# Performance work log

Hardware: AMD Instinct MI355X
Metric: run time of the kernel (lower is better)

Reference implementation:

```python
import jax, jax.numpy as jnp
import numpy as np

N_PATIENT = 50000
N_GENE = 20000
N_EDGE = 640000
P_DIM, G_DIM, H, OUT = 64, 32, 128, 8


def setup_inputs() -> dict:
    key = jax.random.key(0)
    ks = jax.random.split(key, 20)
    s = 0.02
    return {
        "x_patient": jax.random.normal(ks[0], (N_PATIENT, P_DIM), jnp.float32),
        "x_gene": jax.random.normal(ks[1], (N_GENE, G_DIM), jnp.float32),
        "edge_index": jax.random.randint(ks[2], (2, N_EDGE), 0, N_GENE, jnp.int32),
        # patient MLP
        "W_p1": jax.random.normal(ks[3], (P_DIM, H), jnp.float32) * s,
        "b_p1": jnp.zeros((H,), jnp.float32),
        "W_p2": jax.random.normal(ks[4], (H, H), jnp.float32) * s,
        "b_p2": jnp.zeros((H,), jnp.float32),
        # gene MLP
        "W_g1": jax.random.normal(ks[5], (G_DIM, H), jnp.float32) * s,
        "b_g1": jnp.zeros((H,), jnp.float32),
        "W_g2": jax.random.normal(ks[6], (H, H), jnp.float32) * s,
        "b_g2": jnp.zeros((H,), jnp.float32),
        # SAGEConv 1: lin_l acts on aggregated src, lin_r (root) on dst
        "W1_l": jax.random.normal(ks[7], (H, H), jnp.float32) * s,
        "b1_l": jnp.zeros((H,), jnp.float32),
        "W1_r": jax.random.normal(ks[8], (H, H), jnp.float32) * s,
        # SAGEConv 2
        "W2_l": jax.random.normal(ks[9], (H, H), jnp.float32) * s,
        "b2_l": jnp.zeros((H,), jnp.float32),
        "W2_r": jax.random.normal(ks[10], (H, H), jnp.float32) * s,
        # final fc
        "W_fc": jax.random.normal(ks[11], (H, OUT), jnp.float32) * s,
        "b_fc": jnp.zeros((OUT,), jnp.float32),
    }


def reference(x_patient, x_gene, edge_index,
              W_p1, b_p1, W_p2, b_p2,
              W_g1, b_g1, W_g2, b_g2,
              W1_l, b1_l, W1_r,
              W2_l, b2_l, W2_r,
              W_fc, b_fc):
    # node-type MLPs
    p = jax.nn.relu(x_patient @ W_p1 + b_p1) @ W_p2 + b_p2   # [N_P, H]
    g = jax.nn.relu(x_gene @ W_g1 + b_g1) @ W_g2 + b_g2       # [N_G, H]

    src, dst = edge_index[0], edge_index[1]
    # gene_x is unchanged between layers, so the sum-aggregate is identical
    # for both SAGEConv layers: compute the gather + segment-sum once.
    agg = jax.ops.segment_sum(g[src], dst, num_segments=x_patient.shape[0])  # [N_P, H]

    # SAGEConv(aggr='sum'): out = lin_l(agg) + lin_r(x_dst), bias in lin_l
    p = jax.nn.relu(agg @ W1_l + b1_l + p @ W1_r)
    p = jax.nn.relu(agg @ W2_l + b2_l + p @ W2_r)
    return p @ W_fc + b_fc  # [N_P, OUT]
```

## Files before the change

### kernel.cpp

```cpp
#include <hip/hip_runtime.h>

#define NP 50000
#define NG 20000
#define NE 640000
#define PD 64
#define GD 32
#define HD 128
#define OD 8
#define CAP 96
#define FILLB 125
#define EPB 5120
#define GENE_TILES 313
#define ROW0_NOAGG 20096
#define PAT2B 234
#define SAGE64B 314

using f32x4 = __attribute__((ext_vector_type(4))) float;
using s16x8 = __attribute__((ext_vector_type(8))) short;

__device__ __forceinline__ unsigned short f2bf(float f) {
    union { float f; unsigned u; } v; v.f = f;
    const unsigned r = v.u + 0x7FFFu + ((v.u >> 16) & 1u);
    return (unsigned short)(r >> 16);
}
__device__ __forceinline__ float bfpair_lo(unsigned v) {
    union { unsigned u; float f; } x; x.u = v << 16; return x.f;
}
__device__ __forceinline__ float bfpair_hi(unsigned v) {
    union { unsigned u; float f; } x; x.u = v & 0xFFFF0000u; return x.f;
}

#define TOT_SWZ 112640

__global__ __launch_bounds__(256) void swz_kernel(
    const float* __restrict__ Wp1, const float* __restrict__ Wp2,
    const float* __restrict__ W1l, const float* __restrict__ W1r,
    const float* __restrict__ W2l, const float* __restrict__ W2r,
    const float* __restrict__ Wfc,
    const float* __restrict__ Wg1, const float* __restrict__ Wg2,
    unsigned short* __restrict__ wswz)
{
    const int u = blockIdx.x * 256 + threadIdx.x;
    if (u < TOT_SWZ) {
        const float* src; int K, Nr, doff;
        if      (u <   8192) { src = Wp1; K =  64; Nr = HD; doff = 0; }
        else if (u <  24576) { src = Wp2; K = 128; Nr = HD; doff = 8192; }
        else if (u <  40960) { src = W1l; K = 128; Nr = HD; doff = 24576; }
        else if (u <  57344) { src = W1r; K = 128; Nr = HD; doff = 40960; }
        else if (u <  73728) { src = W2l; K = 128; Nr = HD; doff = 57344; }
        else if (u <  90112) { src = W2r; K = 128; Nr = HD; doff = 73728; }
        else if (u <  92160) { src = Wfc; K = 128; Nr = OD; doff = 90112; }
        else if (u <  96256) { src = Wg1; K =  32; Nr = HD; doff = 92160; }
        else                 { src = Wg2; K = 128; Nr = HD; doff = 96256; }
        const int e  = u - doff;
        const int j  = e & 7;
        const int ln = (e >> 3) & 63;
        const int f  = e >> 9;
        const int KC = K >> 5;
        const int c  = f % KC;
        const int n0 = f / KC;
        const int k  = c * 32 + (ln >> 4) * 8 + j;
        const int n  = n0 * 16 + (ln & 15);
        wswz[u] = f2bf((n < Nr) ? src[k * Nr + n] : 0.f);
    }
}

__global__ __launch_bounds__(256) void mega_kernel(
    const float* __restrict__ xp, const float* __restrict__ xg,
    const unsigned short* __restrict__ wswz,
    const float* __restrict__ bg1, const float* __restrict__ bg2,
    const float* __restrict__ bp1, const float* __restrict__ bp2,
    const float* __restrict__ b1l, const float* __restrict__ b2l,
    const float* __restrict__ bfc,
    const int* __restrict__ ei,
    unsigned short* __restrict__ g, int* __restrict__ hist,
    float* __restrict__ out)
{
    __shared__ __align__(16) char smem[40960];
    const int bid = blockIdx.x;
    const int tid = threadIdx.x;

    if (bid >= PAT2B + GENE_TILES) {
        int* cnt = (int*)smem;
#pragma unroll
        for (int k = 0; k < 10; ++k) {
            const int idx = k * 256 + tid;
            if (idx < NG / 8) ((int4*)cnt)[idx] = (int4){0, 0, 0, 0};
        }
        __syncthreads();
        const int fb = bid - PAT2B - GENE_TILES;
        const int base = fb * EPB;
#pragma unroll
        for (int it = 0; it < 5; ++it) {
            const int e0 = base + it * 1024 + tid;
            const int d0 = ei[NE + e0];
            const int d1 = ei[NE + e0 + 256];
            const int d2 = ei[NE + e0 + 512];
            const int d3 = ei[NE + e0 + 768];
            atomicAdd(&cnt[d0 >> 1], 1 << ((d0 & 1) * 16));
            atomicAdd(&cnt[d1 >> 1], 1 << ((d1 & 1) * 16));
            atomicAdd(&cnt[d2 >> 1], 1 << ((d2 & 1) * 16));
            atomicAdd(&cnt[d3 >> 1], 1 << ((d3 & 1) * 16));
        }
        __syncthreads();
        int* Hb = hist + fb * NG;
#pragma unroll
        for (int k = 0; k < 40; ++k) {
            const int idx = k * 256 + tid;
            if (idx < NG / 2) {
                const unsigned w = (unsigned)cnt[idx];
                ((int2*)Hb)[idx] = (int2){(int)(w & 0xFFFFu), (int)(w >> 16)};
            }
        }
        return;
    }

    const int lane = tid & 63;
    const int wid  = tid >> 6;
    const int quad = lane >> 4;
    const int l16  = lane & 15;
    const f32x4 Z = {0.f, 0.f, 0.f, 0.f};

    if (bid >= PAT2B) {
        const unsigned short* wg1 = wswz + 92160;
        const unsigned short* wg2 = wswz + 96256;
        const int row0 = (bid - PAT2B) * 64 + wid * 16;
        const int arow = min(row0 + l16, NG - 1);
        unsigned short* X = (unsigned short*)smem + wid * 16 * 136;

        s16x8 a;
        {
            const float* xr = xg + (size_t)arow * GD + quad * 8;
            const f32x4 u0 = *(const f32x4*)xr;
            const f32x4 u1 = *(const f32x4*)(xr + 4);
#pragma unroll
            for (int j = 0; j < 4; ++j) {
                a[j]     = (short)f2bf(u0[j]);
                a[4 + j] = (short)f2bf(u1[j]);
            }
        }
        f32x4 C[8];
#pragma unroll
        for (int n = 0; n < 8; ++n) {
            const s16x8 b = *(const s16x8*)&wg1[(n * 64 + lane) * 8];
            C[n] = __builtin_amdgcn_mfma_f32_16x16x32_bf16(a, b, Z, 0, 0, 0);
        }
#pragma unroll
        for (int n = 0; n < 8; ++n) {
            const float bias = bg1[n * 16 + l16];
#pragma unroll
            for (int r = 0; r < 4; ++r)
                X[(quad * 4 + r) * 136 + n * 16 + l16] = f2bf(fmaxf(C[n][r] + bias, 0.f));
        }
        __syncthreads();
        s16x8 pa[4];
#pragma unroll
        for (int c = 0; c < 4; ++c) pa[c] = *(const s16x8*)&X[l16 * 136 + c * 32 + quad * 8];
#pragma unroll
        for (int n = 0; n < 8; ++n) {
            C[n] = Z;
#pragma unroll
            for (int c = 0; c < 4; ++c) {
                const s16x8 b = *(const s16x8*)&wg2[((n * 4 + c) * 64 + lane) * 8];
                C[n] = __builtin_amdgcn_mfma_f32_16x16x32_bf16(pa[c], b, C[n], 0, 0, 0);
            }
        }
#pragma unroll
        for (int n = 0; n < 8; ++n) {
            const float bias = bg2[n * 16 + l16];
#pragma unroll
            for (int r = 0; r < 4; ++r) {
                const int row = row0 + quad * 4 + r;
                if (row < NG) g[(size_t)row * HD + n * 16 + l16] = f2bf(C[n][r] + bias);
            }
        }
        return;
    }

    const unsigned short* wp1 = wswz + 0;
    const unsigned short* wp2 = wswz + 8192;
    const unsigned short* w1r = wswz + 40960;
    const unsigned short* w2r = wswz + 73728;
    const unsigned short* wfc = wswz + 90112;

    unsigned short* XA = (unsigned short*)smem;
    const int brow = ROW0_NOAGG + bid * 128;
    const int nA = wid * 2, nB = wid * 2 + 1;

#pragma unroll
    for (int s = 0; s < 8; ++s) {
        const int slot = s * 256 + tid;
        const int r  = slot >> 4;
        const int cv = slot & 15;
        const f32x4 u = *(const f32x4*)&xp[(size_t)min(brow + r, NP - 1) * PD + cv * 4];
        unsigned short o[4];
#pragma unroll
        for (int j = 0; j < 4; ++j) o[j] = f2bf(u[j]);
        *(ushort4*)&XA[r * 136 + cv * 4] = *(ushort4*)o;
    }
    __syncthreads();

    f32x4 acc[8][2];

#pragma unroll
    for (int rt = 0; rt < 8; ++rt) { acc[rt][0] = Z; acc[rt][1] = Z; }
#pragma unroll
    for (int c = 0; c < 2; ++c) {
        const s16x8 b0 = *(const s16x8*)&wp1[((nA * 2 + c) * 64 + lane) * 8];
        const s16x8 b1 = *(const s16x8*)&wp1[((nB * 2 + c) * 64 + lane) * 8];
#pragma unroll
        for (int rt = 0; rt < 8; ++rt) {
            const s16x8 a = *(const s16x8*)&XA[(rt * 16 + l16) * 136 + c * 32 + quad * 8];
            acc[rt][0] = __builtin_amdgcn_mfma_f32_16x16x32_bf16(a, b0, acc[rt][0], 0, 0, 0);
            acc[rt][1] = __builtin_amdgcn_mfma_f32_16x16x32_bf16(a, b1, acc[rt][1], 0, 0, 0);
        }
    }
    __syncthreads();
#pragma unroll
    for (int t = 0; t < 2; ++t) {
        const int n = wid * 2 + t;
        const float bias = bp1[n * 16 + l16];
#pragma unroll
        for (int rt = 0; rt < 8; ++rt)
#pragma unroll
            for (int r = 0; r < 4; ++r)
                XA[(rt * 16 + quad * 4 + r) * 136 + n * 16 + l16] =
                    f2bf(fmaxf(acc[rt][t][r] + bias, 0.f));
    }
    __syncthreads();

#pragma unroll
    for (int rt = 0; rt < 8; ++rt) { acc[rt][0] = Z; acc[rt][1] = Z; }
#pragma unroll
    for (int c = 0; c < 4; ++c) {
        const s16x8 b0 = *(const s16x8*)&wp2[((nA * 4 + c) * 64 + lane) * 8];
        const s16x8 b1 = *(const s16x8*)&wp2[((nB * 4 + c) * 64 + lane) * 8];
#pragma unroll
        for (int rt = 0; rt < 8; ++rt) {
            const s16x8 a = *(const s16x8*)&XA[(rt * 16 + l16) * 136 + c * 32 + quad * 8];
            acc[rt][0] = __builtin_amdgcn_mfma_f32_16x16x32_bf16(a, b0, acc[rt][0], 0, 0, 0);
            acc[rt][1] = __builtin_amdgcn_mfma_f32_16x16x32_bf16(a, b1, acc[rt][1], 0, 0, 0);
        }
    }
    __syncthreads();
#pragma unroll
    for (int t = 0; t < 2; ++t) {
        const int n = wid * 2 + t;
        const float bias = bp2[n * 16 + l16];
#pragma unroll
        for (int rt = 0; rt < 8; ++rt)
#pragma unroll
            for (int r = 0; r < 4; ++r)
                XA[(rt * 16 + quad * 4 + r) * 136 + n * 16 + l16] =
                    f2bf(acc[rt][t][r] + bias);
    }
    __syncthreads();

#pragma unroll
    for (int rt = 0; rt < 8; ++rt) { acc[rt][0] = Z; acc[rt][1] = Z; }
#pragma unroll
    for (int c = 0; c < 4; ++c) {
        const s16x8 b0 = *(const s16x8*)&w1r[((nA * 4 + c) * 64 + lane) * 8];
        const s16x8 b1 = *(const s16x8*)&w1r[((nB * 4 + c) * 64 + lane) * 8];
#pragma unroll
        for (int rt = 0; rt < 8; ++rt) {
            const s16x8 a = *(const s16x8*)&XA[(rt * 16 + l16) * 136 + c * 32 + quad * 8];
            acc[rt][0] = __builtin_amdgcn_mfma_f32_16x16x32_bf16(a, b0, acc[rt][0], 0, 0, 0);
            acc[rt][1] = __builtin_amdgcn_mfma_f32_16x16x32_bf16(a, b1, acc[rt][1], 0, 0, 0);
        }
    }
    __syncthreads();
#pragma unroll
    for (int t = 0; t < 2; ++t) {
        const int n = wid * 2 + t;
        const float bias = b1l[n * 16 + l16];
#pragma unroll
        for (int rt = 0; rt < 8; ++rt)
#pragma unroll
            for (int r = 0; r < 4; ++r)
                XA[(rt * 16 + quad * 4 + r) * 136 + n * 16 + l16] =
                    f2bf(fmaxf(acc[rt][t][r] + bias, 0.f));
    }
    __syncthreads();

#pragma unroll
    for (int rt = 0; rt < 8; ++rt) { acc[rt][0] = Z; acc[rt][1] = Z; }
#pragma unroll
    for (int c = 0; c < 4; ++c) {
        const s16x8 b0 = *(const s16x8*)&w2r[((nA * 4 + c) * 64 + lane) * 8];
        const s16x8 b1 = *(const s16x8*)&w2r[((nB * 4 + c) * 64 + lane) * 8];
#pragma unroll
        for (int rt = 0; rt < 8; ++rt) {
            const s16x8 a = *(const s16x8*)&XA[(rt * 16 + l16) * 136 + c * 32 + quad * 8];
            acc[rt][0] = __builtin_amdgcn_mfma_f32_16x16x32_bf16(a, b0, acc[rt][0], 0, 0, 0);
            acc[rt][1] = __builtin_amdgcn_mfma_f32_16x16x32_bf16(a, b1, acc[rt][1], 0, 0, 0);
        }
    }
    __syncthreads();
#pragma unroll
    for (int t = 0; t < 2; ++t) {
        const int n = wid * 2 + t;
        const float bias = b2l[n * 16 + l16];
#pragma unroll
        for (int rt = 0; rt < 8; ++rt)
#pragma unroll
            for (int r = 0; r < 4; ++r)
                XA[(rt * 16 + quad * 4 + r) * 136 + n * 16 + l16] =
                    f2bf(fmaxf(acc[rt][t][r] + bias, 0.f));
    }
    __syncthreads();

    {
        f32x4 co[2] = {Z, Z};
#pragma unroll
        for (int c = 0; c < 4; ++c) {
            const s16x8 b = *(const s16x8*)&wfc[(c * 64 + lane) * 8];
#pragma unroll
            for (int j = 0; j < 2; ++j) {
                const int rt = wid * 2 + j;
                const s16x8 a = *(const s16x8*)&XA[(rt * 16 + l16) * 136 + c * 32 + quad * 8];
                co[j] = __builtin_amdgcn_mfma_f32_16x16x32_bf16(a, b, co[j], 0, 0, 0);
            }
        }
        if (l16 < OD) {
            const float bias = bfc[l16];
#pragma unroll
            for (int j = 0; j < 2; ++j)
#pragma unroll
                for (int r = 0; r < 4; ++r) {
                    const int row = brow + (wid * 2 + j) * 16 + quad * 4 + r;
                    if (row < NP) out[(size_t)row * OD + l16] = co[j][r] + bias;
                }
        }
    }
}

__global__ __launch_bounds__(256) void scan_kernel(
    int* __restrict__ hist, int* __restrict__ cursor)
{
    const int d = blockIdx.x * 256 + threadIdx.x;
    if (d >= NG) return;
    int run = 0;
#pragma unroll 5
    for (int b = 0; b < FILLB; ++b) {
        const int t = hist[b * NG + d];
        hist[b * NG + d] = run;
        run += t;
    }
    cursor[d] = run;
}

__global__ __launch_bounds__(256) void place_kernel(
    const int* __restrict__ ei, const int* __restrict__ hist,
    unsigned short* __restrict__ pad)
{
    __shared__ __align__(16) int cnt[NG];
    const int tid = threadIdx.x;
    const int* Hb = hist + blockIdx.x * NG;
#pragma unroll
    for (int k = 0; k < 20; ++k) {
        const int idx = k * 256 + tid;
        if (idx < NG / 4) ((int4*)cnt)[idx] = ((const int4*)Hb)[idx];
    }
    __syncthreads();
    const int base = blockIdx.x * EPB;
#pragma unroll
    for (int it = 0; it < 5; ++it) {
        const int e0 = base + it * 1024 + tid;
        const int s0 = ei[e0];       const int d0 = ei[NE + e0];
        const int s1 = ei[e0 + 256]; const int d1 = ei[NE + e0 + 256];
        const int s2 = ei[e0 + 512]; const int d2 = ei[NE + e0 + 512];
        const int s3 = ei[e0 + 768]; const int d3 = ei[NE + e0 + 768];
        { const int p = atomicAdd(&cnt[d0], 1); if (p < CAP) pad[d0 * CAP + p] = (unsigned short)s0; }
        { const int p = atomicAdd(&cnt[d1], 1); if (p < CAP) pad[d1 * CAP + p] = (unsigned short)s1; }
        { const int p = atomicAdd(&cnt[d2], 1); if (p < CAP) pad[d2 * CAP + p] = (unsigned short)s2; }
        { const int p = atomicAdd(&cnt[d3], 1); if (p < CAP) pad[d3 * CAP + p] = (unsigned short)s3; }
    }
}

__global__ __launch_bounds__(256) void agg_kernel(
    const int* __restrict__ cursor, const unsigned short* __restrict__ pad,
    const unsigned short* __restrict__ g, unsigned short* __restrict__ aggb)
{
    const int row  = blockIdx.x * 4 + (threadIdx.x >> 6);
    const int lane = threadIdx.x & 63;
    const int grp  = lane >> 4;
    const int sub  = lane & 15;

    float acc[8] = {0.f, 0.f, 0.f, 0.f, 0.f, 0.f, 0.f, 0.f};
    const int cnt = min(cursor[row], CAP);
    const size_t rb = (size_t)row * CAP;
    for (int i = grp * 4; i < cnt; i += 16) {
        const ushort4 q = *(const ushort4*)&pad[rb + i];
        int r0 = q.x, r1 = q.y, r2 = q.z, r3 = q.w;
        const bool v1 = (i + 1) < cnt, v2 = (i + 2) < cnt, v3 = (i + 3) < cnt;
        r1 = v1 ? r1 : r0;  r2 = v2 ? r2 : r0;  r3 = v3 ? r3 : r0;
        const float s1 = v1 ? 1.f : 0.f, s2 = v2 ? 1.f : 0.f, s3 = v3 ? 1.f : 0.f;
        const s16x8 g0 = *(const s16x8*)&g[(size_t)r0 * HD + sub * 8];
        const s16x8 g1 = *(const s16x8*)&g[(size_t)r1 * HD + sub * 8];
        const s16x8 g2 = *(const s16x8*)&g[(size_t)r2 * HD + sub * 8];
        const s16x8 g3 = *(const s16x8*)&g[(size_t)r3 * HD + sub * 8];
        const unsigned* d0 = (const unsigned*)&g0;
        const unsigned* d1 = (const unsigned*)&g1;
        const unsigned* d2 = (const unsigned*)&g2;
        const unsigned* d3 = (const unsigned*)&g3;
#pragma unroll
        for (int k = 0; k < 4; ++k) {
            acc[2 * k]     += bfpair_lo(d0[k]);
            acc[2 * k + 1] += bfpair_hi(d0[k]);
            acc[2 * k]     = fmaf(bfpair_lo(d1[k]), s1, acc[2 * k]);
            acc[2 * k + 1] = fmaf(bfpair_hi(d1[k]), s1, acc[2 * k + 1]);
            acc[2 * k]     = fmaf(bfpair_lo(d2[k]), s2, acc[2 * k]);
            acc[2 * k + 1] = fmaf(bfpair_hi(d2[k]), s2, acc[2 * k + 1]);
            acc[2 * k]     = fmaf(bfpair_lo(d3[k]), s3, acc[2 * k]);
            acc[2 * k + 1] = fmaf(bfpair_hi(d3[k]), s3, acc[2 * k + 1]);
        }
    }
#pragma unroll
    for (int k = 0; k < 8; ++k) {
        acc[k] += __shfl_xor(acc[k], 16);
        acc[k] += __shfl_xor(acc[k], 32);
    }
    if (lane < 16) {
        unsigned o[4];
#pragma unroll
        for (int k = 0; k < 4; ++k)
            o[k] = (unsigned)f2bf(acc[2 * k]) | ((unsigned)f2bf(acc[2 * k + 1]) << 16);
        *(int4*)&aggb[(size_t)row * HD + lane * 8] = *(int4*)o;
    }
}

__global__ __launch_bounds__(256) void sage64_kernel(
    const float* __restrict__ xp, const unsigned short* __restrict__ aggb,
    const unsigned short* __restrict__ wswz,
    const float* __restrict__ bp1, const float* __restrict__ bp2,
    const float* __restrict__ b1l, const float* __restrict__ b2l,
    const float* __restrict__ bfc,
    float* __restrict__ out)
{
    const unsigned short* wp1 = wswz + 0;
    const unsigned short* wp2 = wswz + 8192;
    const unsigned short* w1l = wswz + 24576;
    const unsigned short* w1r = wswz + 40960;
    const unsigned short* w2l = wswz + 57344;
    const unsigned short* w2r = wswz + 73728;
    const unsigned short* wfc = wswz + 90112;

    __shared__ __align__(16) unsigned short XA[64 * 136];
    __shared__ __align__(16) unsigned short AG[64 * 136];

    const int tid  = threadIdx.x;
    const int lane = tid & 63;
    const int wid  = tid >> 6;
    const int quad = lane >> 4;
    const int l16  = lane & 15;
    const int brow = blockIdx.x * 64;
    const int nA = wid * 2, nB = wid * 2 + 1;
    const f32x4 Z = {0.f, 0.f, 0.f, 0.f};

#pragma unroll
    for (int s = 0; s < 4; ++s) {
        const int slot = s * 256 + tid;
        const int r  = slot >> 4;
        const int cv = slot & 15;
        const f32x4 u = *(const f32x4*)&xp[(size_t)(brow + r) * PD + cv * 4];
        unsigned short o[4];
#pragma unroll
        for (int j = 0; j < 4; ++j) o[j] = f2bf(u[j]);
        *(ushort4*)&XA[r * 136 + cv * 4] = *(ushort4*)o;
    }
#pragma unroll
    for (int s = 0; s < 4; ++s) {
        const int slot = s * 256 + tid;
        const int r  = slot >> 4;
        const int cv = slot & 15;
        const int gr = brow + r;
        s16x8 v = {0, 0, 0, 0, 0, 0, 0, 0};
        if (gr < NG) v = *(const s16x8*)&aggb[(size_t)gr * HD + cv * 8];
        *(s16x8*)&AG[r * 136 + cv * 8] = v;
    }
    __syncthreads();

    f32x4 acc[4][2];

#pragma unroll
    for (int rt = 0; rt < 4; ++rt) { acc[rt][0] = Z; acc[rt][1] = Z; }
#pragma unroll
    for (int c = 0; c < 2; ++c) {
        const s16x8 b0 = *(const s16x8*)&wp1[((nA * 2 + c) * 64 + lane) * 8];
        const s16x8 b1 = *(const s16x8*)&wp1[((nB * 2 + c) * 64 + lane) * 8];
#pragma unroll
        for (int rt = 0; rt < 4; ++rt) {
            const s16x8 a = *(const s16x8*)&XA[(rt * 16 + l16) * 136 + c * 32 + quad * 8];
            acc[rt][0] = __builtin_amdgcn_mfma_f32_16x16x32_bf16(a, b0, acc[rt][0], 0, 0, 0);
            acc[rt][1] = __builtin_amdgcn_mfma_f32_16x16x32_bf16(a, b1, acc[rt][1], 0, 0, 0);
        }
    }
    __syncthreads();
#pragma unroll
    for (int t = 0; t < 2; ++t) {
        const int n = wid * 2 + t;
        const float bias = bp1[n * 16 + l16];
#pragma unroll
        for (int rt = 0; rt < 4; ++rt)
#pragma unroll
            for (int r = 0; r < 4; ++r)
                XA[(rt * 16 + quad * 4 + r) * 136 + n * 16 + l16] =
                    f2bf(fmaxf(acc[rt][t][r] + bias, 0.f));
    }
    __syncthreads();

#pragma unroll
    for (int rt = 0; rt < 4; ++rt) { acc[rt][0] = Z; acc[rt][1] = Z; }
#pragma unroll
    for (int c = 0; c < 4; ++c) {
        const s16x8 b0 = *(const s16x8*)&wp2[((nA * 4 + c) * 64 + lane) * 8];
        const s16x8 b1 = *(const s16x8*)&wp2[((nB * 4 + c) * 64 + lane) * 8];
#pragma unroll
        for (int rt = 0; rt < 4; ++rt) {
            const s16x8 a = *(const s16x8*)&XA[(rt * 16 + l16) * 136 + c * 32 + quad * 8];
            acc[rt][0] = __builtin_amdgcn_mfma_f32_16x16x32_bf16(a, b0, acc[rt][0], 0, 0, 0);
            acc[rt][1] = __builtin_amdgcn_mfma_f32_16x16x32_bf16(a, b1, acc[rt][1], 0, 0, 0);
        }
    }
    __syncthreads();
#pragma unroll
    for (int t = 0; t < 2; ++t) {
        const int n = wid * 2 + t;
        const float bias = bp2[n * 16 + l16];
#pragma unroll
        for (int rt = 0; rt < 4; ++rt)
#pragma unroll
            for (int r = 0; r < 4; ++r)
                XA[(rt * 16 + quad * 4 + r) * 136 + n * 16 + l16] =
                    f2bf(acc[rt][t][r] + bias);
    }
    __syncthreads();

#pragma unroll
    for (int rt = 0; rt < 4; ++rt) { acc[rt][0] = Z; acc[rt][1] = Z; }
#pragma unroll
    for (int c = 0; c < 4; ++c) {
        const s16x8 br0 = *(const s16x8*)&w1r[((nA * 4 + c) * 64 + lane) * 8];
        const s16x8 br1 = *(const s16x8*)&w1r[((nB * 4 + c) * 64 + lane) * 8];
        const s16x8 bl0 = *(const s16x8*)&w1l[((nA * 4 + c) * 64 + lane) * 8];
        const s16x8 bl1 = *(const s16x8*)&w1l[((nB * 4 + c) * 64 + lane) * 8];
#pragma unroll
        for (int rt = 0; rt < 4; ++rt) {
            const s16x8 ap = *(const s16x8*)&XA[(rt * 16 + l16) * 136 + c * 32 + quad * 8];
            const s16x8 ag = *(const s16x8*)&AG[(rt * 16 + l16) * 136 + c * 32 + quad * 8];
            acc[rt][0] = __builtin_amdgcn_mfma_f32_16x16x32_bf16(ap, br0, acc[rt][0], 0, 0, 0);
            acc[rt][0] = __builtin_amdgcn_mfma_f32_16x16x32_bf16(ag, bl0, acc[rt][0], 0, 0, 0);
            acc[rt][1] = __builtin_amdgcn_mfma_f32_16x16x32_bf16(ap, br1, acc[rt][1], 0, 0, 0);
            acc[rt][1] = __builtin_amdgcn_mfma_f32_16x16x32_bf16(ag, bl1, acc[rt][1], 0, 0, 0);
        }
    }
    __syncthreads();
#pragma unroll
    for (int t = 0; t < 2; ++t) {
        const int n = wid * 2 + t;
        const float bias = b1l[n * 16 + l16];
#pragma unroll
        for (int rt = 0; rt < 4; ++rt)
#pragma unroll
            for (int r = 0; r < 4; ++r)
                XA[(rt * 16 + quad * 4 + r) * 136 + n * 16 + l16] =
                    f2bf(fmaxf(acc[rt][t][r] + bias, 0.f));
    }
    __syncthreads();

#pragma unroll
    for (int rt = 0; rt < 4; ++rt) { acc[rt][0] = Z; acc[rt][1] = Z; }
#pragma unroll
    for (int c = 0; c < 4; ++c) {
        const s16x8 br0 = *(const s16x8*)&w2r[((nA * 4 + c) * 64 + lane) * 8];
        const s16x8 br1 = *(const s16x8*)&w2r[((nB * 4 + c) * 64 + lane) * 8];
        const s16x8 bl0 = *(const s16x8*)&w2l[((nA * 4 + c) * 64 + lane) * 8];
        const s16x8 bl1 = *(const s16x8*)&w2l[((nB * 4 + c) * 64 + lane) * 8];
#pragma unroll
        for (int rt = 0; rt < 4; ++rt) {
            const s16x8 ap = *(const s16x8*)&XA[(rt * 16 + l16) * 136 + c * 32 + quad * 8];
            const s16x8 ag = *(const s16x8*)&AG[(rt * 16 + l16) * 136 + c * 32 + quad * 8];
            acc[rt][0] = __builtin_amdgcn_mfma_f32_16x16x32_bf16(ap, br0, acc[rt][0], 0, 0, 0);
            acc[rt][0] = __builtin_amdgcn_mfma_f32_16x16x32_bf16(ag, bl0, acc[rt][0], 0, 0, 0);
            acc[rt][1] = __builtin_amdgcn_mfma_f32_16x16x32_bf16(ap, br1, acc[rt][1], 0, 0, 0);
            acc[rt][1] = __builtin_amdgcn_mfma_f32_16x16x32_bf16(ag, bl1, acc[rt][1], 0, 0, 0);
        }
    }
    __syncthreads();
#pragma unroll
    for (int t = 0; t < 2; ++t) {
        const int n = wid * 2 + t;
        const float bias = b2l[n * 16 + l16];
#pragma unroll
        for (int rt = 0; rt < 4; ++rt)
#pragma unroll
            for (int r = 0; r < 4; ++r)
                XA[(rt * 16 + quad * 4 + r) * 136 + n * 16 + l16] =
                    f2bf(fmaxf(acc[rt][t][r] + bias, 0.f));
    }
    __syncthreads();

    {
        f32x4 co = Z;
#pragma unroll
        for (int c = 0; c < 4; ++c) {
            const s16x8 b = *(const s16x8*)&wfc[(c * 64 + lane) * 8];
            const s16x8 a = *(const s16x8*)&XA[(wid * 16 + l16) * 136 + c * 32 + quad * 8];
            co = __builtin_amdgcn_mfma_f32_16x16x32_bf16(a, b, co, 0, 0, 0);
        }
        if (l16 < OD) {
            const float bias = bfc[l16];
#pragma unroll
            for (int r = 0; r < 4; ++r) {
                const int row = brow + wid * 16 + quad * 4 + r;
                out[(size_t)row * OD + l16] = co[r] + bias;
            }
        }
    }
}

extern "C" void kernel_launch(void* const* d_in, const int* in_sizes, int n_in,
                              void* d_out, int out_size, void* d_ws, size_t ws_size,
                              hipStream_t stream)
{
    const float* xp  = (const float*)d_in[0];
    const float* xg  = (const float*)d_in[1];
    const int*   ei  = (const int*)d_in[2];
    const float* Wp1 = (const float*)d_in[3];
    const float* bp1 = (const float*)d_in[4];
    const float* Wp2 = (const float*)d_in[5];
    const float* bp2 = (const float*)d_in[6];
    const float* Wg1 = (const float*)d_in[7];
    const float* bg1 = (const float*)d_in[8];
    const float* Wg2 = (const float*)d_in[9];
    const float* bg2 = (const float*)d_in[10];
    const float* W1l = (const float*)d_in[11];
    const float* b1l = (const float*)d_in[12];
    const float* W1r = (const float*)d_in[13];
    const float* W2l = (const float*)d_in[14];
    const float* b2l = (const float*)d_in[15];
    const float* W2r = (const float*)d_in[16];
    const float* Wfc = (const float*)d_in[17];
    const float* bfc = (const float*)d_in[18];
    float* out = (float*)d_out;

    char* ws = (char*)d_ws;
    unsigned short* g_b   = (unsigned short*)(ws + 0);
    unsigned short* wswz  = (unsigned short*)(ws + 5120000);
    int*            cursor= (int*)(ws + 5345280);
    int*            hist  = (int*)(ws + 5425280);
    unsigned short* pad   = (unsigned short*)(ws + 15425280);
    unsigned short* agg_b = (unsigned short*)(ws + 19265280);

    swz_kernel<<<(TOT_SWZ + 255) / 256, 256, 0, stream>>>(
        Wp1, Wp2, W1l, W1r, W2l, W2r, Wfc, Wg1, Wg2, wswz);

    mega_kernel<<<PAT2B + GENE_TILES + FILLB, 256, 0, stream>>>(
        xp, xg, wswz, bg1, bg2, bp1, bp2, b1l, b2l, bfc, ei, g_b, hist, out);

    scan_kernel<<<(NG + 255) / 256, 256, 0, stream>>>(hist, cursor);

    place_kernel<<<FILLB, 256, 0, stream>>>(ei, hist, pad);

    agg_kernel<<<NG / 4, 256, 0, stream>>>(cursor, pad, g_b, agg_b);

    sage64_kernel<<<SAGE64B, 256, 0, stream>>>(
        xp, agg_b, wswz, bp1, bp2, b1l, b2l, bfc, out);
}
```

Before: 174.8 us.

## Restructure pipeline: 16-bit histograms, merge place with patient MLP, read agg directly

Splits the old mega kernel so gene MLP and histogram fill run together, while the no-aggregation patient blocks now share a launch with the edge placement kernel. Histograms shrink to 16-bit entries with 8-bit packed shared counters, which halves workspace traffic for the scan and place passes. sage64 drops its shared-memory aggregate staging and reads agg rows from global memory inside the MFMA loop. Padding rows past NG are zeroed in the swizzle kernel. The 8-bit per-block counters assume no node gets more than 255 edges in one 5120-edge block, and the direct global loads may add latency to the inner loop.

```diff
diff --git a/kernel.cpp b/kernel.cpp
--- a/kernel.cpp
+++ b/kernel.cpp
@@ -14,6 +14,7 @@
 #define ROW0_NOAGG 20096
 #define PAT2B 234
 #define SAGE64B 314
+#define AGGPAD (ROW0_NOAGG - NG)
 
 using f32x4 = __attribute__((ext_vector_type(4))) float;
 using s16x8 = __attribute__((ext_vector_type(8))) short;
@@ -38,7 +39,7 @@
     const float* __restrict__ W2l, const float* __restrict__ W2r,
     const float* __restrict__ Wfc,
     const float* __restrict__ Wg1, const float* __restrict__ Wg2,
-    unsigned short* __restrict__ wswz)
+    unsigned short* __restrict__ wswz, unsigned short* __restrict__ aggb)
 {
     const int u = blockIdx.x * 256 + threadIdx.x;
     if (u < TOT_SWZ) {
@@ -62,33 +63,29 @@
         const int k  = c * 32 + (ln >> 4) * 8 + j;
         const int n  = n0 * 16 + (ln & 15);
         wswz[u] = f2bf((n < Nr) ? src[k * Nr + n] : 0.f);
-    }
-}
-
-__global__ __launch_bounds__(256) void mega_kernel(
-    const float* __restrict__ xp, const float* __restrict__ xg,
+    } else {
+        aggb[(size_t)NG * HD + (u - TOT_SWZ)] = 0;
+    }
+}
+
+__global__ __launch_bounds__(256) void genefill_kernel(
+    const float* __restrict__ xg,
     const unsigned short* __restrict__ wswz,
     const float* __restrict__ bg1, const float* __restrict__ bg2,
-    const float* __restrict__ bp1, const float* __restrict__ bp2,
-    const float* __restrict__ b1l, const float* __restrict__ b2l,
-    const float* __restrict__ bfc,
-    const int* __restrict__ ei,
-    unsigned short* __restrict__ g, int* __restrict__ hist,
-    float* __restrict__ out)
+    unsigned short* __restrict__ g,
+    const int* __restrict__ ei, unsigned short* __restrict__ hist16)
 {
-    __shared__ __align__(16) char smem[40960];
-    const int bid = blockIdx.x;
+    __shared__ __align__(16) char smem[20480];
     const int tid = threadIdx.x;
-
-    if (bid >= PAT2B + GENE_TILES) {
+    if (blockIdx.x >= GENE_TILES) {
         int* cnt = (int*)smem;
 #pragma unroll
-        for (int k = 0; k < 10; ++k) {
+        for (int k = 0; k < 5; ++k) {
             const int idx = k * 256 + tid;
-            if (idx < NG / 8) ((int4*)cnt)[idx] = (int4){0, 0, 0, 0};
+            if (idx < NG / 16) ((int4*)cnt)[idx] = (int4){0, 0, 0, 0};
         }
         __syncthreads();
-        const int fb = bid - PAT2B - GENE_TILES;
+        const int fb = blockIdx.x - GENE_TILES;
         const int base = fb * EPB;
 #pragma unroll
         for (int it = 0; it < 5; ++it) {
@@ -97,82 +94,142 @@
             const int d1 = ei[NE + e0 + 256];
             const int d2 = ei[NE + e0 + 512];
             const int d3 = ei[NE + e0 + 768];
-            atomicAdd(&cnt[d0 >> 1], 1 << ((d0 & 1) * 16));
-            atomicAdd(&cnt[d1 >> 1], 1 << ((d1 & 1) * 16));
-            atomicAdd(&cnt[d2 >> 1], 1 << ((d2 & 1) * 16));
-            atomicAdd(&cnt[d3 >> 1], 1 << ((d3 & 1) * 16));
+            atomicAdd(&cnt[d0 >> 2], 1 << ((d0 & 3) * 8));
+            atomicAdd(&cnt[d1 >> 2], 1 << ((d1 & 3) * 8));
+            atomicAdd(&cnt[d2 >> 2], 1 << ((d2 & 3) * 8));
+            atomicAdd(&cnt[d3 >> 2], 1 << ((d3 & 3) * 8));
         }
         __syncthreads();
-        int* Hb = hist + fb * NG;
-#pragma unroll
-        for (int k = 0; k < 40; ++k) {
+        unsigned short* Hb = hist16 + fb * NG;
+#pragma unroll
+        for (int k = 0; k < 20; ++k) {
             const int idx = k * 256 + tid;
-            if (idx < NG / 2) {
+            if (idx < NG / 4) {
                 const unsigned w = (unsigned)cnt[idx];
-                ((int2*)Hb)[idx] = (int2){(int)(w & 0xFFFFu), (int)(w >> 16)};
+                int2 o;
+                o.x = (int)((w & 0xFFu) | ((w & 0xFF00u) << 8));
+                o.y = (int)(((w >> 16) & 0xFFu) | (((w >> 24) & 0xFFu) << 16));
+                ((int2*)Hb)[idx] = o;
             }
         }
         return;
     }
+    const unsigned short* wg1 = wswz + 92160;
+    const unsigned short* wg2 = wswz + 96256;
 
     const int lane = tid & 63;
     const int wid  = tid >> 6;
     const int quad = lane >> 4;
     const int l16  = lane & 15;
+    const int row0 = blockIdx.x * 64 + wid * 16;
+    const int arow = min(row0 + l16, NG - 1);
+    unsigned short* X = (unsigned short*)smem + wid * 16 * 136;
     const f32x4 Z = {0.f, 0.f, 0.f, 0.f};
 
-    if (bid >= PAT2B) {
-        const unsigned short* wg1 = wswz + 92160;
-        const unsigned short* wg2 = wswz + 96256;
-        const int row0 = (bid - PAT2B) * 64 + wid * 16;
-        const int arow = min(row0 + l16, NG - 1);
-        unsigned short* X = (unsigned short*)smem + wid * 16 * 136;
-
-        s16x8 a;
-        {
-            const float* xr = xg + (size_t)arow * GD + quad * 8;
-            const f32x4 u0 = *(const f32x4*)xr;
-            const f32x4 u1 = *(const f32x4*)(xr + 4);
-#pragma unroll
-            for (int j = 0; j < 4; ++j) {
-                a[j]     = (short)f2bf(u0[j]);
-                a[4 + j] = (short)f2bf(u1[j]);
-            }
-        }
-        f32x4 C[8];
-#pragma unroll
-        for (int n = 0; n < 8; ++n) {
-            const s16x8 b = *(const s16x8*)&wg1[(n * 64 + lane) * 8];
-            C[n] = __builtin_amdgcn_mfma_f32_16x16x32_bf16(a, b, Z, 0, 0, 0);
-        }
-#pragma unroll
-        for (int n = 0; n < 8; ++n) {
-            const float bias = bg1[n * 16 + l16];
-#pragma unroll
-            for (int r = 0; r < 4; ++r)
-                X[(quad * 4 + r) * 136 + n * 16 + l16] = f2bf(fmaxf(C[n][r] + bias, 0.f));
+    s16x8 a;
+    {
+        const float* xr = xg + (size_t)arow * GD + quad * 8;
+        const f32x4 u0 = *(const f32x4*)xr;
+        const f32x4 u1 = *(const f32x4*)(xr + 4);
+#pragma unroll
+        for (int j = 0; j < 4; ++j) {
+            a[j]     = (short)f2bf(u0[j]);
+            a[4 + j] = (short)f2bf(u1[j]);
+        }
+    }
+    f32x4 C[8];
+#pragma unroll
+    for (int n = 0; n < 8; ++n) {
+        const s16x8 b = *(const s16x8*)&wg1[(n * 64 + lane) * 8];
+        C[n] = __builtin_amdgcn_mfma_f32_16x16x32_bf16(a, b, Z, 0, 0, 0);
+    }
+#pragma unroll
+    for (int n = 0; n < 8; ++n) {
+        const float bias = bg1[n * 16 + l16];
+#pragma unroll
+        for (int r = 0; r < 4; ++r)
+            X[(quad * 4 + r) * 136 + n * 16 + l16] = f2bf(fmaxf(C[n][r] + bias, 0.f));
+    }
+    __syncthreads();
+    s16x8 pa[4];
+#pragma unroll
+    for (int c = 0; c < 4; ++c) pa[c] = *(const s16x8*)&X[l16 * 136 + c * 32 + quad * 8];
+#pragma unroll
+    for (int n = 0; n < 8; ++n) {
+        C[n] = Z;
+#pragma unroll
+        for (int c = 0; c < 4; ++c) {
+            const s16x8 b = *(const s16x8*)&wg2[((n * 4 + c) * 64 + lane) * 8];
+            C[n] = __builtin_amdgcn_mfma_f32_16x16x32_bf16(pa[c], b, C[n], 0, 0, 0);
+        }
+    }
+#pragma unroll
+    for (int n = 0; n < 8; ++n) {
+        const float bias = bg2[n * 16 + l16];
+#pragma unroll
+        for (int r = 0; r < 4; ++r) {
+            const int row = row0 + quad * 4 + r;
+            if (row < NG) g[(size_t)row * HD + n * 16 + l16] = f2bf(C[n][r] + bias);
+        }
+    }
+}
+
+__global__ __launch_bounds__(256) void scan_kernel(
+    unsigned short* __restrict__ hist16, int* __restrict__ cursor)
+{
+    const int d = blockIdx.x * 256 + threadIdx.x;
+    if (d >= NG) return;
+    int run = 0;
+#pragma unroll 5
+    for (int b = 0; b < FILLB; ++b) {
+        const int t = hist16[b * NG + d];
+        hist16[b * NG + d] = (unsigned short)run;
+        run += t;
+    }
+    cursor[d] = run;
+}
+
+__global__ __launch_bounds__(256) void placepat_kernel(
+    const int* __restrict__ ei, const unsigned short* __restrict__ hist16,
+    unsigned short* __restrict__ pad,
+    const float* __restrict__ xp, const unsigned short* __restrict__ wswz,
+    const float* __restrict__ bp1, const float* __restrict__ bp2,
+    const float* __restrict__ b1l, const float* __restrict__ b2l,
+    const float* __restrict__ bfc,
+    float* __restrict__ out)
+{
+    __shared__ __align__(16) char smem[40960];
+    const int tid = threadIdx.x;
+
+    if (blockIdx.x < FILLB) {
+        int* cnt = (int*)smem;
+        const int* Hb = (const int*)(hist16 + blockIdx.x * NG);
+#pragma unroll
+        for (int k = 0; k < 10; ++k) {
+            const int idx = k * 256 + tid;
+            if (idx < NG / 8) ((int4*)cnt)[idx] = ((const int4*)Hb)[idx];
         }
         __syncthreads();
-        s16x8 pa[4];
-#pragma unroll
-        for (int c = 0; c < 4; ++c) pa[c] = *(const s16x8*)&X[l16 * 136 + c * 32 + quad * 8];
-#pragma unroll
-        for (int n = 0; n < 8; ++n) {
-            C[n] = Z;
-#pragma unroll
-            for (int c = 0; c < 4; ++c) {
-                const s16x8 b = *(const s16x8*)&wg2[((n * 4 + c) * 64 + lane) * 8];
-                C[n] = __builtin_amdgcn_mfma_f32_16x16x32_bf16(pa[c], b, C[n], 0, 0, 0);
-            }
-        }
-#pragma unroll
-        for (int n = 0; n < 8; ++n) {
-            const float bias = bg2[n * 16 + l16];
-#pragma unroll
-            for (int r = 0; r < 4; ++r) {
-                const int row = row0 + quad * 4 + r;
-                if (row < NG) g[(size_t)row * HD + n * 16 + l16] = f2bf(C[n][r] + bias);
-            }
+        const int base = blockIdx.x * EPB;
+#pragma unroll
+        for (int it = 0; it < 5; ++it) {
+            const int e0 = base + it * 1024 + tid;
+            const int s0 = ei[e0];       const int d0 = ei[NE + e0];
+            const int s1 = ei[e0 + 256]; const int d1 = ei[NE + e0 + 256];
+            const int s2 = ei[e0 + 512]; const int d2 = ei[NE + e0 + 512];
+            const int s3 = ei[e0 + 768]; const int d3 = ei[NE + e0 + 768];
+            { const int o = atomicAdd(&cnt[d0 >> 1], 1 << ((d0 & 1) * 16));
+              const int p = (o >> ((d0 & 1) * 16)) & 0xFFFF;
+              if (p < CAP) pad[d0 * CAP + p] = (unsigned short)s0; }
+            { const int o = atomicAdd(&cnt[d1 >> 1], 1 << ((d1 & 1) * 16));
+              const int p = (o >> ((d1 & 1) * 16)) & 0xFFFF;
+              if (p < CAP) pad[d1 * CAP + p] = (unsigned short)s1; }
+            { const int o = atomicAdd(&cnt[d2 >> 1], 1 << ((d2 & 1) * 16));
+              const int p = (o >> ((d2 & 1) * 16)) & 0xFFFF;
+              if (p < CAP) pad[d2 * CAP + p] = (unsigned short)s2; }
+            { const int o = atomicAdd(&cnt[d3 >> 1], 1 << ((d3 & 1) * 16));
+              const int p = (o >> ((d3 & 1) * 16)) & 0xFFFF;
+              if (p < CAP) pad[d3 * CAP + p] = (unsigned short)s3; }
         }
         return;
     }
@@ -184,8 +241,13 @@
     const unsigned short* wfc = wswz + 90112;
 
     unsigned short* XA = (unsigned short*)smem;
-    const int brow = ROW0_NOAGG + bid * 128;
+    const int lane = tid & 63;
+    const int wid  = tid >> 6;
+    const int quad = lane >> 4;
+    const int l16  = lane & 15;
+    const int brow = ROW0_NOAGG + (blockIdx.x - FILLB) * 128;
     const int nA = wid * 2, nB = wid * 2 + 1;
+    const f32x4 Z = {0.f, 0.f, 0.f, 0.f};
 
 #pragma unroll
     for (int s = 0; s < 8; ++s) {
@@ -332,49 +394,6 @@
                     if (row < NP) out[(size_t)row * OD + l16] = co[j][r] + bias;
                 }
         }
-    }
-}
-
-__global__ __launch_bounds__(256) void scan_kernel(
-    int* __restrict__ hist, int* __restrict__ cursor)
-{
-    const int d = blockIdx.x * 256 + threadIdx.x;
-    if (d >= NG) return;
-    int run = 0;
-#pragma unroll 5
-    for (int b = 0; b < FILLB; ++b) {
-        const int t = hist[b * NG + d];
-        hist[b * NG + d] = run;
-        run += t;
-    }
-    cursor[d] = run;
-}
-
-__global__ __launch_bounds__(256) void place_kernel(
-    const int* __restrict__ ei, const int* __restrict__ hist,
-    unsigned short* __restrict__ pad)
-{
-    __shared__ __align__(16) int cnt[NG];
-    const int tid = threadIdx.x;
-    const int* Hb = hist + blockIdx.x * NG;
-#pragma unroll
-    for (int k = 0; k < 20; ++k) {
-        const int idx = k * 256 + tid;
-        if (idx < NG / 4) ((int4*)cnt)[idx] = ((const int4*)Hb)[idx];
-    }
-    __syncthreads();
-    const int base = blockIdx.x * EPB;
-#pragma unroll
-    for (int it = 0; it < 5; ++it) {
-        const int e0 = base + it * 1024 + tid;
-        const int s0 = ei[e0];       const int d0 = ei[NE + e0];
-        const int s1 = ei[e0 + 256]; const int d1 = ei[NE + e0 + 256];
-        const int s2 = ei[e0 + 512]; const int d2 = ei[NE + e0 + 512];
-        const int s3 = ei[e0 + 768]; const int d3 = ei[NE + e0 + 768];
-        { const int p = atomicAdd(&cnt[d0], 1); if (p < CAP) pad[d0 * CAP + p] = (unsigned short)s0; }
-        { const int p = atomicAdd(&cnt[d1], 1); if (p < CAP) pad[d1 * CAP + p] = (unsigned short)s1; }
-        { const int p = atomicAdd(&cnt[d2], 1); if (p < CAP) pad[d2 * CAP + p] = (unsigned short)s2; }
-        { const int p = atomicAdd(&cnt[d3], 1); if (p < CAP) pad[d3 * CAP + p] = (unsigned short)s3; }
     }
 }
 
@@ -447,7 +466,6 @@
     const unsigned short* wfc = wswz + 90112;
 
     __shared__ __align__(16) unsigned short XA[64 * 136];
-    __shared__ __align__(16) unsigned short AG[64 * 136];
 
     const int tid  = threadIdx.x;
     const int lane = tid & 63;
@@ -469,16 +487,6 @@
         for (int j = 0; j < 4; ++j) o[j] = f2bf(u[j]);
         *(ushort4*)&XA[r * 136 + cv * 4] = *(ushort4*)o;
     }
-#pragma unroll
-    for (int s = 0; s < 4; ++s) {
-        const int slot = s * 256 + tid;
-        const int r  = slot >> 4;
-        const int cv = slot & 15;
-        const int gr = brow + r;
-        s16x8 v = {0, 0, 0, 0, 0, 0, 0, 0};
-        if (gr < NG) v = *(const s16x8*)&aggb[(size_t)gr * HD + cv * 8];
-        *(s16x8*)&AG[r * 136 + cv * 8] = v;
-    }
     __syncthreads();
 
     f32x4 acc[4][2];
@@ -548,7 +556,7 @@
 #pragma unroll
         for (int rt = 0; rt < 4; ++rt) {
             const s16x8 ap = *(const s16x8*)&XA[(rt * 16 + l16) * 136 + c * 32 + quad * 8];
-            const s16x8 ag = *(const s16x8*)&AG[(rt * 16 + l16) * 136 + c * 32 + quad * 8];
+            const s16x8 ag = *(const s16x8*)&aggb[(size_t)(brow + rt * 16 + l16) * HD + c * 32 + quad * 8];
             acc[rt][0] = __builtin_amdgcn_mfma_f32_16x16x32_bf16(ap, br0, acc[rt][0], 0, 0, 0);
             acc[rt][0] = __builtin_amdgcn_mfma_f32_16x16x32_bf16(ag, bl0, acc[rt][0], 0, 0, 0);
             acc[rt][1] = __builtin_amdgcn_mfma_f32_16x16x32_bf16(ap, br1, acc[rt][1], 0, 0, 0);
@@ -580,7 +588,7 @@
 #pragma unroll
         for (int rt = 0; rt < 4; ++rt) {
             const s16x8 ap = *(const s16x8*)&XA[(rt * 16 + l16) * 136 + c * 32 + quad * 8];
-            const s16x8 ag = *(const s16x8*)&AG[(rt * 16 + l16) * 136 + c * 32 + quad * 8];
+            const s16x8 ag = *(const s16x8*)&aggb[(size_t)(brow + rt * 16 + l16) * HD + c * 32 + quad * 8];
             acc[rt][0] = __builtin_amdgcn_mfma_f32_16x16x32_bf16(ap, br0, acc[rt][0], 0, 0, 0);
             acc[rt][0] = __builtin_amdgcn_mfma_f32_16x16x32_bf16(ag, bl0, acc[rt][0], 0, 0, 0);
             acc[rt][1] = __builtin_amdgcn_mfma_f32_16x16x32_bf16(ap, br1, acc[rt][1], 0, 0, 0);
@@ -646,22 +654,23 @@
     float* out = (float*)d_out;
 
     char* ws = (char*)d_ws;
-    unsigned short* g_b   = (unsigned short*)(ws + 0);
-    unsigned short* wswz  = (unsigned short*)(ws + 5120000);
-    int*            cursor= (int*)(ws + 5345280);
-    int*            hist  = (int*)(ws + 5425280);
-    unsigned short* pad   = (unsigned short*)(ws + 15425280);
-    unsigned short* agg_b = (unsigned short*)(ws + 19265280);
-
-    swz_kernel<<<(TOT_SWZ + 255) / 256, 256, 0, stream>>>(
-        Wp1, Wp2, W1l, W1r, W2l, W2r, Wfc, Wg1, Wg2, wswz);
-
-    mega_kernel<<<PAT2B + GENE_TILES + FILLB, 256, 0, stream>>>(
-        xp, xg, wswz, bg1, bg2, bp1, bp2, b1l, b2l, bfc, ei, g_b, hist, out);
-
-    scan_kernel<<<(NG + 255) / 256, 256, 0, stream>>>(hist, cursor);
-
-    place_kernel<<<FILLB, 256, 0, stream>>>(ei, hist, pad);
+    unsigned short* g_b    = (unsigned short*)(ws + 0);
+    unsigned short* wswz   = (unsigned short*)(ws + 5120000);
+    int*            cursor = (int*)(ws + 5345280);
+    unsigned short* hist16 = (unsigned short*)(ws + 5425280);
+    unsigned short* pad    = (unsigned short*)(ws + 10425280);
+    unsigned short* agg_b  = (unsigned short*)(ws + 14265280);
+
+    swz_kernel<<<(TOT_SWZ + AGGPAD * HD) / 256, 256, 0, stream>>>(
+        Wp1, Wp2, W1l, W1r, W2l, W2r, Wfc, Wg1, Wg2, wswz, agg_b);
+
+    genefill_kernel<<<GENE_TILES + FILLB, 256, 0, stream>>>(
+        xg, wswz, bg1, bg2, g_b, ei, hist16);
+
+    scan_kernel<<<(NG + 255) / 256, 256, 0, stream>>>(hist16, cursor);
+
+    placepat_kernel<<<FILLB + PAT2B, 256, 0, stream>>>(
+        ei, hist16, pad, xp, wswz, bp1, bp2, b1l, b2l, bfc, out);
 
     agg_kernel<<<NG / 4, 256, 0, stream>>>(cursor, pad, g_b, agg_b);
 
```

After: 174.0 us. Within noise of the previous version (-0.4%).
